# Optimization experiments

Hardware: AMD Instinct MI355X
Metric: run time of the kernel (lower is better)

## Reference

```python
import jax, jax.numpy as jnp
import numpy as np
from jax.scipy.special import logsumexp

EPS = 0.05        # sinkhorn entropic blur (geomloss default blur=0.05, p=1 -> eps=blur)
N_ITERS = 10      # fixed sinkhorn iterations
A_W, B_W = 1.0, 1.0  # chamfer / EMD weights (c=0: projectionLoss undefined in source)


def setup_inputs() -> dict:
    key = jax.random.key(0)
    k1, k2 = jax.random.split(key)
    output = jax.random.normal(k1, (16, 2048, 3), dtype=jnp.float32)
    target = jax.random.normal(k2, (16, 2048, 3), dtype=jnp.float32)
    return {"output": output, "target": target}


def _pairwise_sqdist(x, y):
    # x: [B,N,3], y: [B,M,3] -> [B,N,M]
    x2 = jnp.sum(x * x, axis=-1)                      # [B,N]
    y2 = jnp.sum(y * y, axis=-1)                      # [B,M]
    xy = jnp.einsum('bnd,bmd->bnm', x, y)             # [B,N,M]
    return jnp.maximum(x2[:, :, None] + y2[:, None, :] - 2.0 * xy, 1e-12)


def _total_loss(output, target):
    B, N, _ = output.shape
    M = target.shape[1]
    d2 = _pairwise_sqdist(output, target)             # [B,N,M]

    # Chamfer distance: sum of min squared distances in both directions
    chamfer = jnp.sum(jnp.min(d2, axis=2)) + jnp.sum(jnp.min(d2, axis=1))

    # Sinkhorn EMD with p=1 cost (L2 distance), uniform weights, log-domain
    C = jnp.sqrt(d2)                                  # [B,N,M]
    log_mu = jnp.full((B, N), -jnp.log(jnp.float32(N)), dtype=C.dtype)
    log_nu = jnp.full((B, M), -jnp.log(jnp.float32(M)), dtype=C.dtype)
    f = jnp.zeros((B, N), dtype=C.dtype)
    g = jnp.zeros((B, M), dtype=C.dtype)

    def body(carry, _):
        f, g = carry
        # g_j = -eps * LSE_i[(f_i - C_ij)/eps + log_mu_i]
        g = -EPS * logsumexp((f[:, :, None] - C) / EPS + log_mu[:, :, None], axis=1)
        # f_i = -eps * LSE_j[(g_j - C_ij)/eps + log_nu_j]
        f = -EPS * logsumexp((g[:, None, :] - C) / EPS + log_nu[:, None, :], axis=2)
        return (f, g), None

    (f, g), _ = jax.lax.scan(body, (f, g), None, length=N_ITERS)
    mu = jnp.exp(log_mu)
    nu = jnp.exp(log_nu)
    emd = jnp.sum(mu * f, axis=1) + jnp.sum(nu * g, axis=1)   # [B] dual objective
    emd_loss = jnp.sum(emd * jnp.float32(N))

    return A_W * chamfer + B_W * emd_loss


def reference(output, target):
    return _total_loss(output, target)
```

## Files before the change

### kernel.cpp

```cpp
#include <hip/hip_runtime.h>
#include <math.h>

#define NPTS    2048
#define NBATCH  16
#define THREADS 256
#define BLOCKS_PER_BATCH 64
#define ROWS_PER_BLOCK   32
#define ROWS_PER_WAVE    8

typedef __attribute__((ext_vector_type(2))) float f2;

static constexpr float KEPS_L  = 28.853900817779268f;
static constexpr float LOGMU_L = -11.0f;
static constexpr float EPS_LN2 = 0.03465735902799727f;
static constexpr float INV_K2  = 1.2011331562368226e-3f;
static constexpr float CLAMP2  = 8.325475918208669e-10f;

__global__ void pack_pts(const float* __restrict__ a, const float* __restrict__ b,
                         float4* __restrict__ pa, float4* __restrict__ pb) {
  int idx = blockIdx.x * blockDim.x + threadIdx.x;
  if (idx < NBATCH * NPTS) {
    float x = KEPS_L * a[3*idx], y = KEPS_L * a[3*idx+1], z = KEPS_L * a[3*idx+2];
    pa[idx] = make_float4(x, y, z, fmaf(x, x, fmaf(y, y, z*z)));
    float u = KEPS_L * b[3*idx], v = KEPS_L * b[3*idx+1], w = KEPS_L * b[3*idx+2];
    pb[idx] = make_float4(u, v, w, fmaf(u, u, fmaf(v, v, w*w)));
  }
}

template<bool INIT, bool CHAMFER>
__global__ __launch_bounds__(THREADS, 4)
void lse_pass(const float4* __restrict__ pR, const float4* __restrict__ pQ,
              const float* __restrict__ dualR, float* __restrict__ dualQ,
              float* __restrict__ chamPart) {
  __shared__ float4 sx[NPTS];
  __shared__ float  sw[NPTS];

  const int b    = blockIdx.x >> 6;
  const int blk  = blockIdx.x & 63;
  const int tid  = threadIdx.x;
  const int lane = tid & 63;
  const int wave = tid >> 6;

  const float4* __restrict__ px = pR + b * NPTS;
  float A;

  if constexpr (INIT) {
#pragma unroll
    for (int u = 0; u < 8; ++u) {
      int k = tid + u * THREADS;
      float4 p = px[k];
      sx[k] = make_float4(p.x, p.y, p.z, -0.5f * p.w);
      sw[k] = 1.0f;
    }
    A = LOGMU_L;
    __syncthreads();
  } else {
    const float* __restrict__ fb = dualR + b * NPTS;
    float av[8];
    float lm = -3.4e38f;
#pragma unroll
    for (int u = 0; u < 8; ++u) {
      int k = tid + u * THREADS;
      float a = fmaf(fb[k], KEPS_L, LOGMU_L);
      av[u] = a;
      lm = fmaxf(lm, a);
    }
#pragma unroll
    for (int off = 32; off; off >>= 1) lm = fmaxf(lm, __shfl_xor(lm, off));
    float* scratch = (float*)sx;
    if (lane == 0) scratch[wave] = lm;
    __syncthreads();
    A = fmaxf(fmaxf(scratch[0], scratch[1]), fmaxf(scratch[2], scratch[3]));
    __syncthreads();
#pragma unroll
    for (int u = 0; u < 8; ++u) {
      int k = tid + u * THREADS;
      float4 p = px[k];
      sx[k] = make_float4(p.x, p.y, p.z, -0.5f * p.w);
      sw[k] = __builtin_amdgcn_exp2f(av[u] - A);
    }
    __syncthreads();
  }

  const float4* __restrict__ qa = pQ + b * NPTS;
  float* __restrict__ gout = dualQ + b * NPTS;
  const int j0 = blk * ROWS_PER_BLOCK + wave * ROWS_PER_WAVE;

  f2 qx[4], qy[4], qz[4], qw[4], s2[4], m2[4];
#pragma unroll
  for (int rp = 0; rp < 4; ++rp) {
    float4 q0 = qa[j0 + 2*rp];
    float4 q1 = qa[j0 + 2*rp + 1];
    qx[rp] = (f2){q0.x, q1.x};
    qy[rp] = (f2){q0.y, q1.y};
    qz[rp] = (f2){q0.z, q1.z};
    qw[rp] = (f2){q0.w, q1.w};
    s2[rp] = (f2){0.f, 0.f};
    if constexpr (CHAMFER) m2[rp] = (f2){3.4e38f, 3.4e38f};
  }

  float4 p  = sx[lane];
  float  wi = sw[lane];
  for (int it = 0; it < NPTS / 64; ++it) {
    const int inext = (lane + (it + 1) * 64) & (NPTS - 1);
    const float4 pn = sx[inext];
    const float  wn = sw[inext];
    const f2 pxx = (f2){p.x, p.x};
    const f2 pyy = (f2){p.y, p.y};
    const f2 pzz = (f2){p.z, p.z};
    const f2 pww = (f2){p.w, p.w};
    const f2 wii = (f2){wi, wi};
#pragma unroll
    for (int rp = 0; rp < 4; ++rp) {
      f2 t  = __builtin_elementwise_fma(pxx, qx[rp],
              __builtin_elementwise_fma(pyy, qy[rp],
              __builtin_elementwise_fma(pzz, qz[rp], pww)));
      f2 d2 = __builtin_elementwise_fma((f2){-2.f, -2.f}, t, qw[rp]);
      d2 = __builtin_elementwise_max(d2, (f2){CLAMP2, CLAMP2});
      if constexpr (CHAMFER) m2[rp] = __builtin_elementwise_min(m2[rp], d2);
      float e0 = __builtin_amdgcn_exp2f(-__builtin_amdgcn_sqrtf(d2.x));
      float e1 = __builtin_amdgcn_exp2f(-__builtin_amdgcn_sqrtf(d2.y));
      s2[rp] = __builtin_elementwise_fma((f2){e0, e1}, wii, s2[rp]);
    }
    p = pn;
    wi = wn;
  }

  float s[ROWS_PER_WAVE], m[ROWS_PER_WAVE];
#pragma unroll
  for (int rp = 0; rp < 4; ++rp) {
    s[2*rp] = s2[rp].x;  s[2*rp+1] = s2[rp].y;
    if constexpr (CHAMFER) { m[2*rp] = m2[rp].x;  m[2*rp+1] = m2[rp].y; }
  }

#pragma unroll
  for (int off = 32; off; off >>= 1) {
#pragma unroll
    for (int r = 0; r < ROWS_PER_WAVE; ++r) {
      s[r] += __shfl_xor(s[r], off);
      if constexpr (CHAMFER) m[r] = fminf(m[r], __shfl_xor(m[r], off));
    }
  }

  if (lane == 0) {
#pragma unroll
    for (int r = 0; r < ROWS_PER_WAVE; ++r)
      gout[j0 + r] = -EPS_LN2 * (A + __builtin_amdgcn_logf(fmaxf(s[r], 1e-37f)));
  }

  if constexpr (CHAMFER) {
    float chamAcc = 0.f;
#pragma unroll
    for (int r = 0; r < ROWS_PER_WAVE; ++r) chamAcc += m[r];
    chamAcc *= INV_K2;
    __syncthreads();
    float* scratch = (float*)sx;
    if (lane == 0) scratch[wave] = chamAcc;
    __syncthreads();
    if (tid == 0)
      chamPart[blockIdx.x] = (scratch[0] + scratch[1]) + (scratch[2] + scratch[3]);
  }
}

__global__ void final1(const float4* __restrict__ base, float* __restrict__ part) {
  __shared__ float red[4];
  const int idx = blockIdx.x * THREADS + threadIdx.x;
  float4 v = base[idx];
  float acc = (v.x + v.y) + (v.z + v.w);
#pragma unroll
  for (int off = 32; off; off >>= 1) acc += __shfl_xor(acc, off);
  const int lane = threadIdx.x & 63, wave = threadIdx.x >> 6;
  if (lane == 0) red[wave] = acc;
  __syncthreads();
  if (threadIdx.x == 0) part[blockIdx.x] = (red[0] + red[1]) + (red[2] + red[3]);
}

__global__ void final2(const float* __restrict__ part, float* __restrict__ out) {
  const int lane = threadIdx.x;
  float acc = part[lane];
  if (lane < 2) acc += part[lane + 64];
#pragma unroll
  for (int off = 32; off; off >>= 1) acc += __shfl_xor(acc, off);
  if (lane == 0) out[0] = acc;
}

extern "C" void kernel_launch(void* const* d_in, const int* in_sizes, int n_in,
                              void* d_out, int out_size, void* d_ws, size_t ws_size,
                              hipStream_t stream) {
  const float* outPts = (const float*)d_in[0];
  const float* tgtPts = (const float*)d_in[1];
  float* out = (float*)d_out;

  char* ws = (char*)d_ws;
  float4* pwA = (float4*)ws;
  float4* pwB = (float4*)(ws + (size_t)NBATCH * NPTS * 16);
  float*  f   = (float*)(ws + (size_t)2 * NBATCH * NPTS * 16);
  float*  g   = f + NBATCH * NPTS;
  float*  cham = g + NBATCH * NPTS;
  float*  part = cham + 2048;

  pack_pts<<<dim3(128), dim3(THREADS), 0, stream>>>(outPts, tgtPts, pwA, pwB);

  const dim3 grid(NBATCH * BLOCKS_PER_BATCH);
  const dim3 blk(THREADS);

  lse_pass<true,  true ><<<grid, blk, 0, stream>>>(pwA, pwB, nullptr, g, cham);
  lse_pass<false, true ><<<grid, blk, 0, stream>>>(pwB, pwA, g, f, cham + 1024);
  for (int t = 1; t < 10; ++t) {
    lse_pass<false, false><<<grid, blk, 0, stream>>>(pwA, pwB, f, g, nullptr);
    lse_pass<false, false><<<grid, blk, 0, stream>>>(pwB, pwA, g, f, nullptr);
  }

  final1<<<dim3(66), blk, 0, stream>>>((const float4*)f, part);
  final2<<<dim3(1), dim3(64), 0, stream>>>(part, out);
}
```

Baseline: 399.5 us.

## Split LSE reduction across two waves per row group with 512-thread blocks

Doubles the block to 512 threads and assigns two waves to each 8-row group, each wave covering half of the 2048 source points. The partial sums and chamfer minima are merged through shared memory by wave 0, which also writes the dual outputs. This doubles the number of resident waves per block to improve latency hiding and occupancy. In exchange it adds an extra shared-memory merge step with barriers, and the launch bounds now request more waves per SIMD, which may pressure registers.

```diff
diff --git a/kernel.cpp b/kernel.cpp
--- a/kernel.cpp
+++ b/kernel.cpp
@@ -3,10 +3,11 @@
 
 #define NPTS    2048
 #define NBATCH  16
-#define THREADS 256
+#define THREADS 512
 #define BLOCKS_PER_BATCH 64
 #define ROWS_PER_BLOCK   32
 #define ROWS_PER_WAVE    8
+#define IHALF   1024
 
 typedef __attribute__((ext_vector_type(2))) float f2;
 
@@ -28,7 +29,7 @@
 }
 
 template<bool INIT, bool CHAMFER>
-__global__ __launch_bounds__(THREADS, 4)
+__global__ __launch_bounds__(THREADS, 8)
 void lse_pass(const float4* __restrict__ pR, const float4* __restrict__ pQ,
               const float* __restrict__ dualR, float* __restrict__ dualQ,
               float* __restrict__ chamPart) {
@@ -40,13 +41,15 @@
   const int tid  = threadIdx.x;
   const int lane = tid & 63;
   const int wave = tid >> 6;
+  const int rg   = wave >> 1;
+  const int half = wave & 1;
 
   const float4* __restrict__ px = pR + b * NPTS;
   float A;
 
   if constexpr (INIT) {
 #pragma unroll
-    for (int u = 0; u < 8; ++u) {
+    for (int u = 0; u < 4; ++u) {
       int k = tid + u * THREADS;
       float4 p = px[k];
       sx[k] = make_float4(p.x, p.y, p.z, -0.5f * p.w);
@@ -56,10 +59,10 @@
     __syncthreads();
   } else {
     const float* __restrict__ fb = dualR + b * NPTS;
-    float av[8];
+    float av[4];
     float lm = -3.4e38f;
 #pragma unroll
-    for (int u = 0; u < 8; ++u) {
+    for (int u = 0; u < 4; ++u) {
       int k = tid + u * THREADS;
       float a = fmaf(fb[k], KEPS_L, LOGMU_L);
       av[u] = a;
@@ -70,10 +73,11 @@
     float* scratch = (float*)sx;
     if (lane == 0) scratch[wave] = lm;
     __syncthreads();
-    A = fmaxf(fmaxf(scratch[0], scratch[1]), fmaxf(scratch[2], scratch[3]));
-    __syncthreads();
-#pragma unroll
-    for (int u = 0; u < 8; ++u) {
+    A = fmaxf(fmaxf(fmaxf(scratch[0], scratch[1]), fmaxf(scratch[2], scratch[3])),
+              fmaxf(fmaxf(scratch[4], scratch[5]), fmaxf(scratch[6], scratch[7])));
+    __syncthreads();
+#pragma unroll
+    for (int u = 0; u < 4; ++u) {
       int k = tid + u * THREADS;
       float4 p = px[k];
       sx[k] = make_float4(p.x, p.y, p.z, -0.5f * p.w);
@@ -84,7 +88,7 @@
 
   const float4* __restrict__ qa = pQ + b * NPTS;
   float* __restrict__ gout = dualQ + b * NPTS;
-  const int j0 = blk * ROWS_PER_BLOCK + wave * ROWS_PER_WAVE;
+  const int j0 = blk * ROWS_PER_BLOCK + rg * ROWS_PER_WAVE;
 
   f2 qx[4], qy[4], qz[4], qw[4], s2[4], m2[4];
 #pragma unroll
@@ -99,10 +103,14 @@
     if constexpr (CHAMFER) m2[rp] = (f2){3.4e38f, 3.4e38f};
   }
 
-  float4 p  = sx[lane];
-  float  wi = sw[lane];
-  for (int it = 0; it < NPTS / 64; ++it) {
-    const int inext = (lane + (it + 1) * 64) & (NPTS - 1);
+  const f2 kM2 = (f2){-2.f, -2.f};
+  const f2 kCl = (f2){CLAMP2, CLAMP2};
+
+  const int base = half * IHALF;
+  float4 p  = sx[base + lane];
+  float  wi = sw[base + lane];
+  for (int it = 0; it < IHALF / 64; ++it) {
+    const int inext = base + ((lane + (it + 1) * 64) & (IHALF - 1));
     const float4 pn = sx[inext];
     const float  wn = sw[inext];
     const f2 pxx = (f2){p.x, p.x};
@@ -115,8 +123,8 @@
       f2 t  = __builtin_elementwise_fma(pxx, qx[rp],
               __builtin_elementwise_fma(pyy, qy[rp],
               __builtin_elementwise_fma(pzz, qz[rp], pww)));
-      f2 d2 = __builtin_elementwise_fma((f2){-2.f, -2.f}, t, qw[rp]);
-      d2 = __builtin_elementwise_max(d2, (f2){CLAMP2, CLAMP2});
+      f2 d2 = __builtin_elementwise_fma(kM2, t, qw[rp]);
+      d2 = __builtin_elementwise_max(d2, kCl);
       if constexpr (CHAMFER) m2[rp] = __builtin_elementwise_min(m2[rp], d2);
       float e0 = __builtin_amdgcn_exp2f(-__builtin_amdgcn_sqrtf(d2.x));
       float e1 = __builtin_amdgcn_exp2f(-__builtin_amdgcn_sqrtf(d2.y));
@@ -142,29 +150,38 @@
     }
   }
 
+  __syncthreads();
+  float* sScr = (float*)sx;
+  float* mScr = sScr + 64;
   if (lane == 0) {
 #pragma unroll
-    for (int r = 0; r < ROWS_PER_WAVE; ++r)
-      gout[j0 + r] = -EPS_LN2 * (A + __builtin_amdgcn_logf(fmaxf(s[r], 1e-37f)));
-  }
-
-  if constexpr (CHAMFER) {
-    float chamAcc = 0.f;
-#pragma unroll
-    for (int r = 0; r < ROWS_PER_WAVE; ++r) chamAcc += m[r];
-    chamAcc *= INV_K2;
-    __syncthreads();
-    float* scratch = (float*)sx;
-    if (lane == 0) scratch[wave] = chamAcc;
-    __syncthreads();
-    if (tid == 0)
-      chamPart[blockIdx.x] = (scratch[0] + scratch[1]) + (scratch[2] + scratch[3]);
+    for (int r = 0; r < ROWS_PER_WAVE; ++r) {
+      sScr[wave * 8 + r] = s[r];
+      if constexpr (CHAMFER) mScr[wave * 8 + r] = m[r];
+    }
+  }
+  __syncthreads();
+
+  if (wave == 0) {
+    float sc = 0.f, mc = 0.f;
+    if (lane < 32) {
+      const int g = lane >> 3, r = lane & 7;
+      sc = sScr[g * 16 + r] + sScr[g * 16 + 8 + r];
+      gout[blk * ROWS_PER_BLOCK + lane] =
+          -EPS_LN2 * (A + __builtin_amdgcn_logf(fmaxf(sc, 1e-37f)));
+      if constexpr (CHAMFER) mc = fminf(mScr[g * 16 + r], mScr[g * 16 + 8 + r]);
+    }
+    if constexpr (CHAMFER) {
+#pragma unroll
+      for (int off = 32; off; off >>= 1) mc += __shfl_xor(mc, off);
+      if (lane == 0) chamPart[blockIdx.x] = mc * INV_K2;
+    }
   }
 }
 
 __global__ void final1(const float4* __restrict__ base, float* __restrict__ part) {
   __shared__ float red[4];
-  const int idx = blockIdx.x * THREADS + threadIdx.x;
+  const int idx = blockIdx.x * 256 + threadIdx.x;
   float4 v = base[idx];
   float acc = (v.x + v.y) + (v.z + v.w);
 #pragma unroll
@@ -199,7 +216,7 @@
   float*  cham = g + NBATCH * NPTS;
   float*  part = cham + 2048;
 
-  pack_pts<<<dim3(128), dim3(THREADS), 0, stream>>>(outPts, tgtPts, pwA, pwB);
+  pack_pts<<<dim3(128), dim3(256), 0, stream>>>(outPts, tgtPts, pwA, pwB);
 
   const dim3 grid(NBATCH * BLOCKS_PER_BATCH);
   const dim3 blk(THREADS);
@@ -211,6 +228,6 @@
     lse_pass<false, false><<<grid, blk, 0, stream>>>(pwB, pwA, g, f, nullptr);
   }
 
-  final1<<<dim3(66), blk, 0, stream>>>((const float4*)f, part);
+  final1<<<dim3(66), dim3(256), 0, stream>>>((const float4*)f, part);
   final2<<<dim3(1), dim3(64), 0, stream>>>(part, out);
 }
```

Result: slower. 427.9 us (median of 2 runs) (+7.1%).
